# Kernel optimization log

Hardware: AMD Instinct MI355X
Metric: run time of the kernel (lower is better)

The kernel has to match this reference:

```python
import jax, jax.numpy as jnp
import numpy as np

N = 50000      # nodes
E = 800000     # edges (before self loops)
D = 128        # embedding_dimension
HEADS = 4
C = 32         # hidden_channels
NEG_SLOPE = 0.2


def setup_inputs() -> dict:
    key = jax.random.key(0)
    ks = jax.random.split(key, 12)
    s = 0.1
    x = jax.random.normal(ks[0], (N, D), jnp.float32)
    edge_index = jax.random.randint(ks[1], (2, E), 0, N)
    # layer 1: D -> HEADS*C, concat
    W1 = jax.random.normal(ks[2], (D, HEADS * C), jnp.float32) * s
    a_src1 = jax.random.normal(ks[3], (HEADS, C), jnp.float32) * s
    a_dst1 = jax.random.normal(ks[4], (HEADS, C), jnp.float32) * s
    b1 = jnp.zeros((HEADS * C,), jnp.float32)
    # layer 2: HEADS*C -> HEADS*C, concat
    W2 = jax.random.normal(ks[5], (HEADS * C, HEADS * C), jnp.float32) * s
    a_src2 = jax.random.normal(ks[6], (HEADS, C), jnp.float32) * s
    a_dst2 = jax.random.normal(ks[7], (HEADS, C), jnp.float32) * s
    b2 = jnp.zeros((HEADS * C,), jnp.float32)
    # layer 3: HEADS*C -> C, heads=1, no concat (mean over the single head)
    W3 = jax.random.normal(ks[8], (HEADS * C, C), jnp.float32) * s
    a_src3 = jax.random.normal(ks[9], (1, C), jnp.float32) * s
    a_dst3 = jax.random.normal(ks[10], (1, C), jnp.float32) * s
    b3 = jnp.zeros((C,), jnp.float32)
    return {"x": x, "edge_index": edge_index,
            "W1": W1, "a_src1": a_src1, "a_dst1": a_dst1, "b1": b1,
            "W2": W2, "a_src2": a_src2, "a_dst2": a_dst2, "b2": b2,
            "W3": W3, "a_src3": a_src3, "a_dst3": a_dst3, "b3": b3}


def gat_layer(x, src, dst, W, a_s, a_d, b, heads, concat):
    """One PyG-style GATConv (eval mode: dropout inactive).
    x: [N, Fin]; src/dst: [E2] (self loops included)."""
    n = x.shape[0]
    h = (x @ W).reshape(n, heads, -1)                 # [N, H, C]
    alpha_src = (h * a_s).sum(-1)                     # [N, H]
    alpha_dst = (h * a_d).sum(-1)                     # [N, H]
    logits = jax.nn.leaky_relu(alpha_src[src] + alpha_dst[dst], NEG_SLOPE)  # [E2, H]
    # segment softmax over destination nodes
    m = jax.ops.segment_max(logits, dst, num_segments=n)          # [N, H]
    ex = jnp.exp(logits - m[dst])                                  # [E2, H]
    denom = jax.ops.segment_sum(ex, dst, num_segments=n)          # [N, H]
    alpha = ex / (denom[dst] + 1e-16)                              # [E2, H]
    msg = h[src] * alpha[:, :, None]                               # [E2, H, C]
    out = jax.ops.segment_sum(msg, dst, num_segments=n)            # [N, H, C]
    if concat:
        return out.reshape(n, -1) + b
    return out.mean(axis=1) + b


def reference(x, edge_index, W1, a_src1, a_dst1, b1, W2, a_src2, a_dst2, b2,
              W3, a_src3, a_dst3, b3):
    loops = jnp.arange(N, dtype=edge_index.dtype)
    src = jnp.concatenate([edge_index[0], loops])   # add_self_loops=True
    dst = jnp.concatenate([edge_index[1], loops])
    h = gat_layer(x, src, dst, W1, a_src1, a_dst1, b1, HEADS, True)
    h = jax.nn.elu(h)
    h = gat_layer(h, src, dst, W2, a_src2, a_dst2, b2, HEADS, True)
    h = jax.nn.elu(h)
    out = gat_layer(h, src, dst, W3, a_src3, a_dst3, b3, 1, False)
    return out
```

## Files before the change

### kernel.cpp

```cpp
#include <hip/hip_runtime.h>
#include <cmath>

constexpr int NN  = 50000;
constexpr int EE  = 800000;
constexpr int E2C = EE + NN;

constexpr int NBUCK = 256;
constexpr int BW    = 196;
constexpr int NCH   = 16;
constexpr int CW    = 3125;
constexpr int EPT   = 8;
constexpr int CH    = 256 * EPT;
constexpr int NB_B  = (E2C + CH - 1) / CH;
constexpr int CAP   = 4096;
constexpr int SCAP  = 5120;
constexpr int G1ALL = (NN + 63) / 64;
constexpr int G1A   = 391;

constexpr float RLN2 = 1.44269504088896340736f;

using bf16x8 = __attribute__((ext_vector_type(8))) short;
using f32x4  = __attribute__((ext_vector_type(4))) float;

__device__ inline unsigned bf16rne(float f) {
    unsigned u = __builtin_bit_cast(unsigned, f);
    return (u + 0x7fffu + ((u >> 16) & 1u)) >> 16;
}
__device__ inline float bflo(unsigned u) { return __builtin_bit_cast(float, u << 16); }
__device__ inline float bfhi(unsigned u) { return __builtin_bit_cast(float, u & 0xffff0000u); }

__global__ __launch_bounds__(256) void cvt_weights(
    const float* __restrict__ W1, const float* __restrict__ W2,
    const float* __restrict__ W3,
    unsigned short* __restrict__ W1t, unsigned short* __restrict__ W2t,
    unsigned short* __restrict__ W3t, int* __restrict__ bcursor,
    float* __restrict__ AS1, float* __restrict__ AS2, float* __restrict__ AS3,
    unsigned short* __restrict__ H1, unsigned short* __restrict__ H2,
    unsigned short* __restrict__ H3)
{
    int g = blockIdx.x * 256 + threadIdx.x;
    if (g < NBUCK) bcursor[g] = 0;
    if (g < 4) { AS1[NN * 4 + g] = -1e30f; AS2[NN * 4 + g] = -1e30f; }
    if (g == 4) AS3[NN] = -1e30f;
    if (g < 128) { H1[(size_t)NN * 128 + g] = 0; H2[(size_t)NN * 128 + g] = 0; }
    if (g < 32)  H3[(size_t)NN * 32 + g] = 0;

    const float* W; unsigned short* Wt; int cols;
    if (g < 2048)      { W = W1; Wt = W1t; cols = 128; }
    else if (g < 4096) { W = W2; Wt = W2t; cols = 128; g -= 2048; }
    else if (g < 4608) { W = W3; Wt = W3t; cols = 32;  g -= 4096; }
    else return;
    int c  = g / 16;
    int k8 = (g % 16) * 8;
    unsigned up[4];
    #pragma unroll
    for (int j = 0; j < 4; ++j) {
        float a = W[(k8 + 2 * j) * cols + c];
        float b = W[(k8 + 2 * j + 1) * cols + c];
        up[j] = bf16rne(a) | (bf16rne(b) << 16);
    }
    uint4 u; u.x = up[0]; u.y = up[1]; u.z = up[2]; u.w = up[3];
    *(uint4*)(Wt + c * 128 + k8) = u;
}

template<int NT, int NH, bool F32IN>
__device__ inline void gemm_body(
    int bid, const void* __restrict__ inv, const unsigned short* __restrict__ Wt,
    const float* __restrict__ a_s, const float* __restrict__ a_d,
    unsigned short* __restrict__ hout, float* __restrict__ asrc,
    float* __restrict__ adst)
{
    constexpr int COLS = NT * 16;
    constexpr int TPH  = NT / NH;
    const int lane = threadIdx.x & 63;
    const int wave = threadIdx.x >> 6;
    const int m    = lane & 15;
    const int quad = lane >> 4;
    const int n0   = bid * 64 + wave * 16;

    int arow = n0 + m; if (arow >= NN) arow = NN - 1;

    f32x4 acc[NT] = {};
    #pragma unroll
    for (int kq = 0; kq < 4; ++kq) {
        bf16x8 a;
        if constexpr (F32IN) {
            const float* ap = (const float*)inv + (long long)arow * 128 + quad * 8 + kq * 32;
            float4 v0 = *(const float4*)ap;
            float4 v1 = *(const float4*)(ap + 4);
            a[0] = (short)bf16rne(v0.x); a[1] = (short)bf16rne(v0.y);
            a[2] = (short)bf16rne(v0.z); a[3] = (short)bf16rne(v0.w);
            a[4] = (short)bf16rne(v1.x); a[5] = (short)bf16rne(v1.y);
            a[6] = (short)bf16rne(v1.z); a[7] = (short)bf16rne(v1.w);
        } else {
            a = *(const bf16x8*)((const unsigned short*)inv
                    + (long long)arow * 128 + quad * 8 + kq * 32);
        }
        #pragma unroll
        for (int t = 0; t < NT; ++t) {
            bf16x8 b = *(const bf16x8*)(Wt + (t * 16 + m) * 128 + kq * 32 + quad * 8);
            acc[t] = __builtin_amdgcn_mfma_f32_16x16x32_bf16(a, b, acc[t], 0, 0, 0);
        }
    }

    #pragma unroll
    for (int r = 0; r < 4; ++r) {
        int node = n0 + quad * 4 + r;
        if (node < NN) {
            #pragma unroll
            for (int t = 0; t < NT; ++t)
                hout[(long long)node * COLS + t * 16 + m] =
                    (unsigned short)bf16rne(acc[t][r]);
        }
    }

    float asv[NT], adv[NT];
    #pragma unroll
    for (int t = 0; t < NT; ++t) {
        asv[t] = a_s[t * 16 + m] * RLN2;
        adv[t] = a_d[t * 16 + m] * RLN2;
    }

    #pragma unroll
    for (int r = 0; r < 4; ++r) {
        const int node = n0 + quad * 4 + r;
        #pragma unroll
        for (int hh = 0; hh < NH; ++hh) {
            float ps = 0.f, pd = 0.f;
            #pragma unroll
            for (int q = 0; q < TPH; ++q) {
                int t = hh * TPH + q;
                ps = fmaf(acc[t][r], asv[t], ps);
                pd = fmaf(acc[t][r], adv[t], pd);
            }
            #pragma unroll
            for (int off = 8; off > 0; off >>= 1) {
                ps += __shfl_down(ps, off, 16);
                pd += __shfl_down(pd, off, 16);
            }
            if (m == 0 && node < NN) {
                asrc[node * NH + hh] = ps;
                adst[node * NH + hh] = pd;
            }
        }
    }
}

__device__ inline void bin_body(
    int bid, const int* __restrict__ ei, int* __restrict__ bcursor,
    unsigned* __restrict__ pairs)
{
    __shared__ int cnt[NBUCK];
    __shared__ int scanex[NBUCK];
    __shared__ int base[NBUCK];
    __shared__ int cur[NBUCK];
    __shared__ unsigned stage[CH];

    const int tid = threadIdx.x;
    const long long e0 = (long long)bid * CH;
    cnt[tid] = 0;
    __syncthreads();

    unsigned rec[EPT]; int bk[EPT];
    #pragma unroll
    for (int j = 0; j < EPT; ++j) {
        long long e = e0 + tid + j * 256;
        bool valid = e < E2C;
        int ss = 0, dd = 0;
        if (valid) {
            if (e < EE) { ss = ei[e]; dd = ei[EE + e]; }
            else        { ss = dd = (int)(e - EE); }
        }
        int b = dd / BW;
        bk[j]  = valid ? b : -1;
        rec[j] = (unsigned)ss | ((unsigned)(dd - b * BW) << 16) | ((unsigned)b << 24);
        if (valid) atomicAdd(&cnt[b], 1);
    }
    __syncthreads();

    const int myc = cnt[tid];
    scanex[tid] = myc;
    __syncthreads();
    for (int off = 1; off < NBUCK; off <<= 1) {
        int t = (tid >= off) ? scanex[tid - off] : 0;
        __syncthreads();
        scanex[tid] += t;
        __syncthreads();
    }
    int excl = scanex[tid] - myc;
    __syncthreads();
    scanex[tid] = excl;
    cur[tid]    = excl;
    base[tid]   = atomicAdd(&bcursor[tid], myc);
    __syncthreads();

    #pragma unroll
    for (int j = 0; j < EPT; ++j) {
        if (bk[j] >= 0) {
            int p = atomicAdd(&cur[bk[j]], 1);
            stage[p] = rec[j];
        }
    }
    __syncthreads();

    const int total = (e0 + CH <= E2C) ? CH : (int)(E2C - e0);
    for (int j = tid; j < total; j += 256) {
        unsigned p = stage[j];
        int b = (int)(p >> 24);
        pairs[(size_t)b * CAP + base[b] + (j - scanex[b])] = p;
    }
}

__device__ inline void sort_body(
    int b, const int* __restrict__ bcursor, const unsigned* __restrict__ pairs,
    int2* __restrict__ rowp, unsigned short* __restrict__ sorted_src,
    unsigned short* __restrict__ perm)
{
    __shared__ int deg[256];
    __shared__ int scn[256];
    __shared__ int cur[256];
    __shared__ int hist2[64];
    __shared__ int scn2[64];
    __shared__ int cur2[64];
    const int n0 = b * BW;
    const int n1 = (n0 + BW < NN) ? n0 + BW : NN;
    const int nloc = n1 - n0;
    const int tid = threadIdx.x;
    const int mycnt = bcursor[b];
    const unsigned* seg = pairs + (size_t)b * CAP;
    const int base = b * SCAP;

    deg[tid] = 0;
    if (tid < 64) hist2[tid] = 0;
    __syncthreads();
    for (int i = tid; i < mycnt; i += 256)
        atomicAdd(&deg[(seg[i] >> 16) & 0xff], 1);
    __syncthreads();

    const int pv = (deg[tid] + 3) & ~3;
    int it = pv >> 2; if (it > 63) it = 63;
    it = 63 - it;
    scn[tid] = pv;
    if (tid < nloc) atomicAdd(&hist2[it], 1);
    __syncthreads();
    for (int off = 1; off < 256; off <<= 1) {
        int t = (tid >= off) ? scn[tid - off] : 0;
        __syncthreads();
        scn[tid] += t;
        __syncthreads();
    }
    if (tid < 64) scn2[tid] = hist2[tid];
    __syncthreads();
    for (int off = 1; off < 64; off <<= 1) {
        int t = (tid >= off && tid < 64) ? scn2[tid - off] : 0;
        __syncthreads();
        if (tid < 64) scn2[tid] += t;
        __syncthreads();
    }
    if (tid < 64) cur2[tid] = scn2[tid] - hist2[tid];
    __syncthreads();

    const int totalp = scn[255];
    const int pexcl  = scn[tid] - pv;
    cur[tid] = base + pexcl;
    if (tid < nloc) {
        int rank = atomicAdd(&cur2[it], 1);
        perm[n0 + rank] = (unsigned short)(n0 + tid);
        rowp[n0 + rank] = make_int2(base + pexcl, base + pexcl + pv);
    }
    __syncthreads();

    int lim = totalp + 8; if (lim > SCAP) lim = SCAP;
    for (int i = tid; i < lim; i += 256)
        sorted_src[base + i] = (unsigned short)NN;
    if (b == NBUCK - 1 && tid < 8)
        sorted_src[NBUCK * SCAP + tid] = (unsigned short)NN;
    __syncthreads();

    for (int c = 0; c < NCH; ++c) {
        const unsigned lo = (unsigned)(c * CW), hi = lo + CW;
        for (int i = tid; i < mycnt; i += 256) {
            unsigned p = seg[i];
            unsigned ss = p & 0xffffu;
            if (ss >= lo && ss < hi) {
                int pos = atomicAdd(&cur[(p >> 16) & 0xff], 1);
                sorted_src[pos] = (unsigned short)ss;
            }
        }
        __syncthreads();
    }
}

__global__ __launch_bounds__(256) void bin_gemm(
    const int* __restrict__ ei, int* __restrict__ bcursor,
    unsigned* __restrict__ pairs,
    const float* __restrict__ x, const unsigned short* __restrict__ Wt,
    const float* __restrict__ a_s, const float* __restrict__ a_d,
    unsigned short* __restrict__ hout, float* __restrict__ asrc,
    float* __restrict__ adst)
{
    if (blockIdx.x < NB_B)
        bin_body(blockIdx.x, ei, bcursor, pairs);
    else
        gemm_body<8, 4, true>(blockIdx.x - NB_B, x, Wt, a_s, a_d, hout, asrc, adst);
}

__global__ __launch_bounds__(256) void sort_gemm(
    const int* __restrict__ bcursor, const unsigned* __restrict__ pairs,
    int2* __restrict__ rowp, unsigned short* __restrict__ sorted_src,
    unsigned short* __restrict__ perm,
    const float* __restrict__ x, const unsigned short* __restrict__ Wt,
    const float* __restrict__ a_s, const float* __restrict__ a_d,
    unsigned short* __restrict__ hout, float* __restrict__ asrc,
    float* __restrict__ adst)
{
    if (blockIdx.x < NBUCK)
        sort_body(blockIdx.x, bcursor, pairs, rowp, sorted_src, perm);
    else
        gemm_body<8, 4, true>(blockIdx.x - NBUCK + G1A, x, Wt, a_s, a_d,
                              hout, asrc, adst);
}

template<int COLS, int NH>
__device__ inline void aggr_range(
    int b0, int e0, int head, float ad,
    const unsigned short* __restrict__ sorted_src,
    const uint* __restrict__ hp,
    const float* __restrict__ asrc,
    float num[8], float& den)
{
    constexpr int USTR = COLS / 2;
    ushort4 sv = *(const ushort4*)&sorted_src[b0];
    for (int i = b0; i < e0; i += 4) {
        ushort4 nx = *(const ushort4*)&sorted_src[i + 4];
        const int s[4] = {sv.x, sv.y, sv.z, sv.w};
        float a[4];
        uint4 Hv[4];
        #pragma unroll
        for (int j = 0; j < 4; ++j) a[j] = asrc[s[j] * NH + head];
        #pragma unroll
        for (int j = 0; j < 4; ++j)
            Hv[j] = *(const uint4*)&hp[(long long)s[j] * USTR];
        #pragma unroll
        for (int j = 0; j < 4; ++j) {
            float l = a[j] + ad; l = l > 0.f ? l : 0.2f * l;
            float w;
            asm("v_exp_f32 %0, %1" : "=v"(w) : "v"(l));
            den += w;
            num[0] = fmaf(w, bflo(Hv[j].x), num[0]); num[1] = fmaf(w, bfhi(Hv[j].x), num[1]);
            num[2] = fmaf(w, bflo(Hv[j].y), num[2]); num[3] = fmaf(w, bfhi(Hv[j].y), num[3]);
            num[4] = fmaf(w, bflo(Hv[j].z), num[4]); num[5] = fmaf(w, bfhi(Hv[j].z), num[5]);
            num[6] = fmaf(w, bflo(Hv[j].w), num[6]); num[7] = fmaf(w, bfhi(Hv[j].w), num[7]);
        }
        sv = nx;
    }
}

template<int NT_OUT, int NH_OUT>
__global__ __launch_bounds__(256) void aggr_gemm(
    const unsigned short* __restrict__ perm,
    const int2* __restrict__ rowp, const unsigned short* __restrict__ sorted_src,
    const unsigned short* __restrict__ hin,
    const float* __restrict__ asrc_in, const float* __restrict__ adst_in,
    const float* __restrict__ bias,
    const unsigned short* __restrict__ Wt,
    const float* __restrict__ a_s, const float* __restrict__ a_d,
    unsigned short* __restrict__ hout, float* __restrict__ asrc_out,
    float* __restrict__ adst_out)
{
    __shared__ unsigned short lds_h[16 * 128];
    __shared__ int lds_node[16];
    const int tid = threadIdx.x;
    const int row = tid >> 4;
    const int lc  = tid & 15;
    const int rk  = blockIdx.x * 16 + row;
    const int d   = perm[rk];
    if (lc == 0) lds_node[row] = d;

    const int cc   = lc * 8;
    const int head = cc / 32;
    const float ad = adst_in[d * 4 + head];
    const uint* hp = (const uint*)hin + cc / 2;
    const int2 be = rowp[rk];

    float num[8] = {};
    float den = 0.f;
    aggr_range<128, 4>(be.x, be.y, head, ad, sorted_src, hp, asrc_in, num, den);

    float inv = 1.f / (den + 1e-16f);
    float v[8];
    #pragma unroll
    for (int j = 0; j < 8; ++j) {
        v[j] = num[j] * inv + bias[cc + j];
        v[j] = v[j] > 0.f ? v[j] : expm1f(v[j]);
    }
    uint4 u;
    u.x = bf16rne(v[0]) | (bf16rne(v[1]) << 16);
    u.y = bf16rne(v[2]) | (bf16rne(v[3]) << 16);
    u.z = bf16rne(v[4]) | (bf16rne(v[5]) << 16);
    u.w = bf16rne(v[6]) | (bf16rne(v[7]) << 16);
    *(uint4*)((char*)lds_h + row * 256 + ((lc * 16) ^ ((row & 7) << 4))) = u;
    __syncthreads();

    const int lane = tid & 63;
    const int wave = tid >> 6;
    const int m    = lane & 15;
    const int quad = lane >> 4;
    int t0;
    if constexpr (NT_OUT == 8) t0 = wave * 2;
    else { if (wave != 0) return; t0 = 0; }

    f32x4 acc[2] = {};
    #pragma unroll
    for (int kq = 0; kq < 4; ++kq) {
        int colb = (quad * 16 + kq * 64) ^ ((m & 7) << 4);
        bf16x8 a = *(const bf16x8*)((const char*)lds_h + m * 256 + colb);
        #pragma unroll
        for (int tt = 0; tt < 2; ++tt) {
            bf16x8 b = *(const bf16x8*)(Wt + ((t0 + tt) * 16 + m) * 128
                                        + kq * 32 + quad * 8);
            acc[tt] = __builtin_amdgcn_mfma_f32_16x16x32_bf16(a, b, acc[tt], 0, 0, 0);
        }
    }

    constexpr int COLS_OUT = NT_OUT * 16;
    const int headw = t0 / (NT_OUT / NH_OUT);
    float asv[2], adv[2];
    #pragma unroll
    for (int tt = 0; tt < 2; ++tt) {
        asv[tt] = a_s[(t0 + tt) * 16 + m] * RLN2;
        adv[tt] = a_d[(t0 + tt) * 16 + m] * RLN2;
    }

    #pragma unroll
    for (int r = 0; r < 4; ++r) {
        const int node = lds_node[quad * 4 + r];
        #pragma unroll
        for (int tt = 0; tt < 2; ++tt)
            hout[(long long)node * COLS_OUT + (t0 + tt) * 16 + m] =
                (unsigned short)bf16rne(acc[tt][r]);
        float ps = acc[0][r] * asv[0];
        ps = fmaf(acc[1][r], asv[1], ps);
        float pd = acc[0][r] * adv[0];
        pd = fmaf(acc[1][r], adv[1], pd);
        #pragma unroll
        for (int off = 8; off > 0; off >>= 1) {
            ps += __shfl_down(ps, off, 16);
            pd += __shfl_down(pd, off, 16);
        }
        if (m == 0) {
            asrc_out[node * NH_OUT + headw] = ps;
            adst_out[node * NH_OUT + headw] = pd;
        }
    }
}

template<int COLS, int NH>
__global__ __launch_bounds__(256) void aggr_final(
    const unsigned short* __restrict__ perm,
    const int2* __restrict__ rowp, const unsigned short* __restrict__ sorted_src,
    const unsigned short* __restrict__ hin,
    const float* __restrict__ asrc, const float* __restrict__ adst,
    const float* __restrict__ bias, float* __restrict__ out)
{
    constexpr int TPN = COLS / 8;
    int t = blockIdx.x * 256 + threadIdx.x;
    int rk = t / TPN;
    int lc = t % TPN;
    if (rk >= NN) return;
    const int d = perm[rk];
    const int cc = lc * 8;
    const int head = cc / 32;
    const float ad = adst[d * NH + head];
    const int2 be = rowp[rk];
    const uint* hp = (const uint*)hin + cc / 2;
    float num[8] = {};
    float den = 0.f;
    aggr_range<COLS, NH>(be.x, be.y, head, ad, sorted_src, hp, asrc, num, den);
    float inv = 1.f / (den + 1e-16f);
    float v[8];
    #pragma unroll
    for (int j = 0; j < 8; ++j) v[j] = num[j] * inv + bias[cc + j];
    float4 o0 = {v[0], v[1], v[2], v[3]};
    float4 o1 = {v[4], v[5], v[6], v[7]};
    *(float4*)&out[(long long)d * COLS + lc * 8]     = o0;
    *(float4*)&out[(long long)d * COLS + lc * 8 + 4] = o1;
}

extern "C" void kernel_launch(void* const* d_in, const int* in_sizes, int n_in,
                              void* d_out, int out_size, void* d_ws, size_t ws_size,
                              hipStream_t stream)
{
    const float* x   = (const float*)d_in[0];
    const int*   ei  = (const int*)  d_in[1];
    const float* W1  = (const float*)d_in[2];
    const float* as1 = (const float*)d_in[3];
    const float* ad1 = (const float*)d_in[4];
    const float* b1  = (const float*)d_in[5];
    const float* W2  = (const float*)d_in[6];
    const float* as2 = (const float*)d_in[7];
    const float* ad2 = (const float*)d_in[8];
    const float* b2  = (const float*)d_in[9];
    const float* W3  = (const float*)d_in[10];
    const float* as3 = (const float*)d_in[11];
    const float* ad3 = (const float*)d_in[12];
    const float* b3  = (const float*)d_in[13];
    float* out = (float*)d_out;

    unsigned short* H1  = (unsigned short*)d_ws;
    unsigned short* H2  = H1 + (size_t)(NN + 1) * 128;
    unsigned short* H3  = H2 + (size_t)(NN + 1) * 128;
    unsigned short* W1t = H3 + (size_t)(NN + 1) * 32;
    unsigned short* W2t = W1t + 128 * 128;
    unsigned short* W3t = W2t + 128 * 128;
    float* AS1 = (float*)(W3t + 32 * 128);
    float* AD1 = AS1 + (size_t)(NN + 1) * 4;
    float* AS2 = AD1 + (size_t)NN * 4;
    float* AD2 = AS2 + (size_t)(NN + 1) * 4;
    float* AS3 = AD2 + (size_t)NN * 4;
    float* AD3 = AS3 + (size_t)(NN + 1);
    int2* rowp = (int2*)(AD3 + NN);
    unsigned short* sorted = (unsigned short*)(rowp + NN);
    int* bcursor = (int*)(sorted + (size_t)NBUCK * SCAP + 8);
    unsigned short* perm = (unsigned short*)(bcursor + NBUCK);
    size_t off = ((size_t)(perm + NN) - (size_t)d_ws + 15) & ~(size_t)15;
    unsigned* pairs = (unsigned*)((char*)d_ws + off);

    const int gCvtW  = (4608 + 255) / 256;
    const int gBinG  = NB_B + G1A;
    const int gSortG = NBUCK + (G1ALL - G1A);
    const int gFused = NN / 16;
    const int gAggr3 = (NN * 4 + 255) / 256;

    cvt_weights<<<gCvtW, 256, 0, stream>>>(W1, W2, W3, W1t, W2t, W3t, bcursor,
                                           AS1, AS2, AS3, H1, H2, H3);
    bin_gemm<<<gBinG, 256, 0, stream>>>(ei, bcursor, pairs,
                                        x, W1t, as1, ad1, H1, AS1, AD1);
    sort_gemm<<<gSortG, 256, 0, stream>>>(bcursor, pairs, rowp, sorted, perm,
                                          x, W1t, as1, ad1, H1, AS1, AD1);
    aggr_gemm<8, 4><<<gFused, 256, 0, stream>>>(
        perm, rowp, sorted, H1, AS1, AD1, b1, W2t, as2, ad2, H2, AS2, AD2);
    aggr_gemm<2, 1><<<gFused, 256, 0, stream>>>(
        perm, rowp, sorted, H2, AS2, AD2, b2, W3t, as3, ad3, H3, AS3, AD3);
    aggr_final<32, 1><<<gAggr3, 256, 0, stream>>>(
        perm, rowp, sorted, H3, AS3, AD3, b3, out);
}
```

Baseline: 284.6 us.

## Use column-sliced feature layout and split aggregation from GEMM

Hidden features are now stored as column slices (16 or 8 columns per slice, each slice holding all nodes). Aggregation kernels then work on one slice per block, so gathered rows are smaller and the working set fits the cache better. The fused aggregate+GEMM kernels are split into separate slice-wise aggregation and standalone GEMM launches. This adds launches and an extra round trip of intermediates through memory. The sort step also drops its chunked multi-pass scatter for a single pass, which changes the order of source indices within each row.

Result: slower. 351.3 us (+23.4%).

```diff
diff --git a/kernel.cpp b/kernel.cpp
--- a/kernel.cpp
+++ b/kernel.cpp
@@ -7,8 +7,6 @@
 
 constexpr int NBUCK = 256;
 constexpr int BW    = 196;
-constexpr int NCH   = 16;
-constexpr int CW    = 3125;
 constexpr int EPT   = 8;
 constexpr int CH    = 256 * EPT;
 constexpr int NB_B  = (E2C + CH - 1) / CH;
@@ -21,6 +19,7 @@
 
 using bf16x8 = __attribute__((ext_vector_type(8))) short;
 using f32x4  = __attribute__((ext_vector_type(4))) float;
+using u32x4  = __attribute__((ext_vector_type(4))) unsigned int;
 
 __device__ inline unsigned bf16rne(float f) {
     unsigned u = __builtin_bit_cast(unsigned, f);
@@ -35,15 +34,19 @@
     unsigned short* __restrict__ W1t, unsigned short* __restrict__ W2t,
     unsigned short* __restrict__ W3t, int* __restrict__ bcursor,
     float* __restrict__ AS1, float* __restrict__ AS2, float* __restrict__ AS3,
-    unsigned short* __restrict__ H1, unsigned short* __restrict__ H2,
+    unsigned short* __restrict__ HA, unsigned short* __restrict__ HB,
     unsigned short* __restrict__ H3)
 {
     int g = blockIdx.x * 256 + threadIdx.x;
     if (g < NBUCK) bcursor[g] = 0;
     if (g < 4) { AS1[NN * 4 + g] = -1e30f; AS2[NN * 4 + g] = -1e30f; }
     if (g == 4) AS3[NN] = -1e30f;
-    if (g < 128) { H1[(size_t)NN * 128 + g] = 0; H2[(size_t)NN * 128 + g] = 0; }
-    if (g < 32)  H3[(size_t)NN * 32 + g] = 0;
+    if (g < 128) {
+        HA[((size_t)(g >> 4) * (NN + 1) + NN) * 16 + (g & 15)] = 0;
+        HB[((size_t)(g >> 4) * (NN + 1) + NN) * 16 + (g & 15)] = 0;
+    }
+    if (g < 32)
+        H3[((size_t)(g >> 3) * (NN + 1) + NN) * 8 + (g & 7)] = 0;
 
     const float* W; unsigned short* Wt; int cols;
     if (g < 2048)      { W = W1; Wt = W1t; cols = 128; }
@@ -63,7 +66,7 @@
     *(uint4*)(Wt + c * 128 + k8) = u;
 }
 
-template<int NT, int NH, bool F32IN>
+template<int NT, int NH, bool F32IN, int GRP_OUT>
 __device__ inline void gemm_body(
     int bid, const void* __restrict__ inv, const unsigned short* __restrict__ Wt,
     const float* __restrict__ a_s, const float* __restrict__ a_d,
@@ -93,8 +96,9 @@
             a[4] = (short)bf16rne(v1.x); a[5] = (short)bf16rne(v1.y);
             a[6] = (short)bf16rne(v1.z); a[7] = (short)bf16rne(v1.w);
         } else {
+            int c = quad * 8 + kq * 32;
             a = *(const bf16x8*)((const unsigned short*)inv
-                    + (long long)arow * 128 + quad * 8 + kq * 32);
+                    + ((size_t)(c >> 4) * (NN + 1) + arow) * 16 + (c & 15));
         }
         #pragma unroll
         for (int t = 0; t < NT; ++t) {
@@ -108,9 +112,15 @@
         int node = n0 + quad * 4 + r;
         if (node < NN) {
             #pragma unroll
-            for (int t = 0; t < NT; ++t)
-                hout[(long long)node * COLS + t * 16 + m] =
-                    (unsigned short)bf16rne(acc[t][r]);
+            for (int t = 0; t < NT; ++t) {
+                int c2 = t * 16 + m;
+                if constexpr (GRP_OUT == 16)
+                    hout[((size_t)(c2 >> 4) * (NN + 1) + node) * 16 + (c2 & 15)] =
+                        (unsigned short)bf16rne(acc[t][r]);
+                else
+                    hout[((size_t)(c2 >> 3) * (NN + 1) + node) * 8 + (c2 & 7)] =
+                        (unsigned short)bf16rne(acc[t][r]);
+            }
         }
     }
 
@@ -276,18 +286,10 @@
     if (b == NBUCK - 1 && tid < 8)
         sorted_src[NBUCK * SCAP + tid] = (unsigned short)NN;
     __syncthreads();
-
-    for (int c = 0; c < NCH; ++c) {
-        const unsigned lo = (unsigned)(c * CW), hi = lo + CW;
-        for (int i = tid; i < mycnt; i += 256) {
-            unsigned p = seg[i];
-            unsigned ss = p & 0xffffu;
-            if (ss >= lo && ss < hi) {
-                int pos = atomicAdd(&cur[(p >> 16) & 0xff], 1);
-                sorted_src[pos] = (unsigned short)ss;
-            }
-        }
-        __syncthreads();
+    for (int i = tid; i < mycnt; i += 256) {
+        unsigned p = seg[i];
+        int pos = atomicAdd(&cur[(p >> 16) & 0xff], 1);
+        sorted_src[pos] = (unsigned short)(p & 0xffff);
     }
 }
 
@@ -302,7 +304,8 @@
     if (blockIdx.x < NB_B)
         bin_body(blockIdx.x, ei, bcursor, pairs);
     else
-        gemm_body<8, 4, true>(blockIdx.x - NB_B, x, Wt, a_s, a_d, hout, asrc, adst);
+        gemm_body<8, 4, true, 16>(blockIdx.x - NB_B, x, Wt, a_s, a_d,
+                                  hout, asrc, adst);
 }
 
 __global__ __launch_bounds__(256) void sort_gemm(
@@ -317,8 +320,26 @@
     if (blockIdx.x < NBUCK)
         sort_body(blockIdx.x, bcursor, pairs, rowp, sorted_src, perm);
     else
-        gemm_body<8, 4, true>(blockIdx.x - NBUCK + G1A, x, Wt, a_s, a_d,
-                              hout, asrc, adst);
+        gemm_body<8, 4, true, 16>(blockIdx.x - NBUCK + G1A, x, Wt, a_s, a_d,
+                                  hout, asrc, adst);
+}
+
+__global__ __launch_bounds__(256) void gemm_l2(
+    const unsigned short* __restrict__ hin, const unsigned short* __restrict__ Wt,
+    const float* __restrict__ a_s, const float* __restrict__ a_d,
+    unsigned short* __restrict__ hout, float* __restrict__ asrc,
+    float* __restrict__ adst)
+{
+    gemm_body<8, 4, false, 16>(blockIdx.x, hin, Wt, a_s, a_d, hout, asrc, adst);
+}
+
+__global__ __launch_bounds__(256) void gemm_l3(
+    const unsigned short* __restrict__ hin, const unsigned short* __restrict__ Wt,
+    const float* __restrict__ a_s, const float* __restrict__ a_d,
+    unsigned short* __restrict__ hout, float* __restrict__ asrc,
+    float* __restrict__ adst)
+{
+    gemm_body<2, 1, false, 8>(blockIdx.x, hin, Wt, a_s, a_d, hout, asrc, adst);
 }
 
 template<int COLS, int NH>
@@ -356,135 +377,76 @@
     }
 }
 
-template<int NT_OUT, int NH_OUT>
-__global__ __launch_bounds__(256) void aggr_gemm(
+__global__ __launch_bounds__(256) void aggr_slice128(
     const unsigned short* __restrict__ perm,
     const int2* __restrict__ rowp, const unsigned short* __restrict__ sorted_src,
     const unsigned short* __restrict__ hin,
-    const float* __restrict__ asrc_in, const float* __restrict__ adst_in,
+    const float* __restrict__ asrc, const float* __restrict__ adst,
     const float* __restrict__ bias,
-    const unsigned short* __restrict__ Wt,
-    const float* __restrict__ a_s, const float* __restrict__ a_d,
-    unsigned short* __restrict__ hout, float* __restrict__ asrc_out,
-    float* __restrict__ adst_out)
-{
-    __shared__ unsigned short lds_h[16 * 128];
-    __shared__ int lds_node[16];
-    const int tid = threadIdx.x;
-    const int row = tid >> 4;
-    const int lc  = tid & 15;
-    const int rk  = blockIdx.x * 16 + row;
-    const int d   = perm[rk];
-    if (lc == 0) lds_node[row] = d;
-
-    const int cc   = lc * 8;
-    const int head = cc / 32;
-    const float ad = adst_in[d * 4 + head];
-    const uint* hp = (const uint*)hin + cc / 2;
-    const int2 be = rowp[rk];
+    unsigned short* __restrict__ outg)
+{
+    const int g    = blockIdx.x & 7;
+    const int ib   = blockIdx.x >> 3;
+    const int tid  = threadIdx.x;
+    const int ln   = tid >> 1;
+    const int half = tid & 1;
+    const int rk   = ib * 128 + ln;
+    if (rk >= NN) return;
+    const int d    = perm[rk];
+    const int head = g >> 1;
+    const float ad = adst[d * 4 + head];
+    const uint* hp = (const uint*)hin + (size_t)g * (NN + 1) * 8 + half * 4;
+    const int2 be  = rowp[rk];
 
     float num[8] = {};
     float den = 0.f;
-    aggr_range<128, 4>(be.x, be.y, head, ad, sorted_src, hp, asrc_in, num, den);
+    aggr_range<16, 4>(be.x, be.y, head, ad, sorted_src, hp, asrc, num, den);
 
     float inv = 1.f / (den + 1e-16f);
+    const int cc = g * 16 + half * 8;
     float v[8];
     #pragma unroll
     for (int j = 0; j < 8; ++j) {
         v[j] = num[j] * inv + bias[cc + j];
         v[j] = v[j] > 0.f ? v[j] : expm1f(v[j]);
     }
-    uint4 u;
-    u.x = bf16rne(v[0]) | (bf16rne(v[1]) << 16);
-    u.y = bf16rne(v[2]) | (bf16rne(v[3]) << 16);
-    u.z = bf16rne(v[4]) | (bf16rne(v[5]) << 16);
-    u.w = bf16rne(v[6]) | (bf16rne(v[7]) << 16);
-    *(uint4*)((char*)lds_h + row * 256 + ((lc * 16) ^ ((row & 7) << 4))) = u;
-    __syncthreads();
-
-    const int lane = tid & 63;
-    const int wave = tid >> 6;
-    const int m    = lane & 15;
-    const int quad = lane >> 4;
-    int t0;
-    if constexpr (NT_OUT == 8) t0 = wave * 2;
-    else { if (wave != 0) return; t0 = 0; }
-
-    f32x4 acc[2] = {};
-    #pragma unroll
-    for (int kq = 0; kq < 4; ++kq) {
-        int colb = (quad * 16 + kq * 64) ^ ((m & 7) << 4);
-        bf16x8 a = *(const bf16x8*)((const char*)lds_h + m * 256 + colb);
-        #pragma unroll
-        for (int tt = 0; tt < 2; ++tt) {
-            bf16x8 b = *(const bf16x8*)(Wt + ((t0 + tt) * 16 + m) * 128
-                                        + kq * 32 + quad * 8);
-            acc[tt] = __builtin_amdgcn_mfma_f32_16x16x32_bf16(a, b, acc[tt], 0, 0, 0);
-        }
-    }
-
-    constexpr int COLS_OUT = NT_OUT * 16;
-    const int headw = t0 / (NT_OUT / NH_OUT);
-    float asv[2], adv[2];
-    #pragma unroll
-    for (int tt = 0; tt < 2; ++tt) {
-        asv[tt] = a_s[(t0 + tt) * 16 + m] * RLN2;
-        adv[tt] = a_d[(t0 + tt) * 16 + m] * RLN2;
-    }
-
-    #pragma unroll
-    for (int r = 0; r < 4; ++r) {
-        const int node = lds_node[quad * 4 + r];
-        #pragma unroll
-        for (int tt = 0; tt < 2; ++tt)
-            hout[(long long)node * COLS_OUT + (t0 + tt) * 16 + m] =
-                (unsigned short)bf16rne(acc[tt][r]);
-        float ps = acc[0][r] * asv[0];
-        ps = fmaf(acc[1][r], asv[1], ps);
-        float pd = acc[0][r] * adv[0];
-        pd = fmaf(acc[1][r], adv[1], pd);
-        #pragma unroll
-        for (int off = 8; off > 0; off >>= 1) {
-            ps += __shfl_down(ps, off, 16);
-            pd += __shfl_down(pd, off, 16);
-        }
-        if (m == 0) {
-            asrc_out[node * NH_OUT + headw] = ps;
-            adst_out[node * NH_OUT + headw] = pd;
-        }
-    }
-}
-
-template<int COLS, int NH>
-__global__ __launch_bounds__(256) void aggr_final(
+    u32x4 u;
+    u[0] = bf16rne(v[0]) | (bf16rne(v[1]) << 16);
+    u[1] = bf16rne(v[2]) | (bf16rne(v[3]) << 16);
+    u[2] = bf16rne(v[4]) | (bf16rne(v[5]) << 16);
+    u[3] = bf16rne(v[6]) | (bf16rne(v[7]) << 16);
+    __builtin_nontemporal_store(
+        u, (u32x4*)(outg + ((size_t)g * (NN + 1) + d) * 16 + half * 8));
+}
+
+__global__ __launch_bounds__(256) void aggr_final_g(
     const unsigned short* __restrict__ perm,
     const int2* __restrict__ rowp, const unsigned short* __restrict__ sorted_src,
     const unsigned short* __restrict__ hin,
     const float* __restrict__ asrc, const float* __restrict__ adst,
     const float* __restrict__ bias, float* __restrict__ out)
 {
-    constexpr int TPN = COLS / 8;
-    int t = blockIdx.x * 256 + threadIdx.x;
-    int rk = t / TPN;
-    int lc = t % TPN;
+    const int g  = blockIdx.x & 3;
+    const int ib = blockIdx.x >> 2;
+    const int rk = ib * 256 + threadIdx.x;
     if (rk >= NN) return;
-    const int d = perm[rk];
-    const int cc = lc * 8;
-    const int head = cc / 32;
-    const float ad = adst[d * NH + head];
-    const int2 be = rowp[rk];
-    const uint* hp = (const uint*)hin + cc / 2;
+    const int d  = perm[rk];
+    const float ad = adst[d];
+    const uint* hp = (const uint*)hin + (size_t)g * (NN + 1) * 4;
+    const int2 be  = rowp[rk];
+
     float num[8] = {};
     float den = 0.f;
-    aggr_range<COLS, NH>(be.x, be.y, head, ad, sorted_src, hp, asrc, num, den);
+    aggr_range<8, 1>(be.x, be.y, 0, ad, sorted_src, hp, asrc, num, den);
+
     float inv = 1.f / (den + 1e-16f);
+    const int cc = g * 8;
     float v[8];
     #pragma unroll
     for (int j = 0; j < 8; ++j) v[j] = num[j] * inv + bias[cc + j];
-    float4 o0 = {v[0], v[1], v[2], v[3]};
-    float4 o1 = {v[4], v[5], v[6], v[7]};
-    *(float4*)&out[(long long)d * COLS + lc * 8]     = o0;
-    *(float4*)&out[(long long)d * COLS + lc * 8 + 4] = o1;
+    float* op = out + (long long)d * 32 + cc;
+    *(float4*)(op)     = make_float4(v[0], v[1], v[2], v[3]);
+    *(float4*)(op + 4) = make_float4(v[4], v[5], v[6], v[7]);
 }
 
 extern "C" void kernel_launch(void* const* d_in, const int* in_sizes, int n_in,
@@ -507,9 +469,9 @@
     const float* b3  = (const float*)d_in[13];
     float* out = (float*)d_out;
 
-    unsigned short* H1  = (unsigned short*)d_ws;
-    unsigned short* H2  = H1 + (size_t)(NN + 1) * 128;
-    unsigned short* H3  = H2 + (size_t)(NN + 1) * 128;
+    unsigned short* HA  = (unsigned short*)d_ws;
+    unsigned short* HB  = HA + (size_t)(NN + 1) * 128;
+    unsigned short* H3  = HB + (size_t)(NN + 1) * 128;
     unsigned short* W1t = H3 + (size_t)(NN + 1) * 32;
     unsigned short* W2t = W1t + 128 * 128;
     unsigned short* W3t = W2t + 128 * 128;
@@ -529,19 +491,22 @@
     const int gCvtW  = (4608 + 255) / 256;
     const int gBinG  = NB_B + G1A;
     const int gSortG = NBUCK + (G1ALL - G1A);
-    const int gFused = NN / 16;
-    const int gAggr3 = (NN * 4 + 255) / 256;
+    const int gGemm  = G1ALL;
+    const int gAggrS = 8 * ((NN + 127) / 128);
+    const int gAggrF = 4 * ((NN + 255) / 256);
 
     cvt_weights<<<gCvtW, 256, 0, stream>>>(W1, W2, W3, W1t, W2t, W3t, bcursor,
-                                           AS1, AS2, AS3, H1, H2, H3);
+                                           AS1, AS2, AS3, HA, HB, H3);
     bin_gemm<<<gBinG, 256, 0, stream>>>(ei, bcursor, pairs,
-                                        x, W1t, as1, ad1, H1, AS1, AD1);
+                                        x, W1t, as1, ad1, HA, AS1, AD1);
     sort_gemm<<<gSortG, 256, 0, stream>>>(bcursor, pairs, rowp, sorted, perm,
-                                          x, W1t, as1, ad1, H1, AS1, AD1);
-    aggr_gemm<8, 4><<<gFused, 256, 0, stream>>>(
-        perm, rowp, sorted, H1, AS1, AD1, b1, W2t, as2, ad2, H2, AS2, AD2);
-    aggr_gemm<2, 1><<<gFused, 256, 0, stream>>>(
-        perm, rowp, sorted, H2, AS2, AD2, b2, W3t, as3, ad3, H3, AS3, AD3);
-    aggr_final<32, 1><<<gAggr3, 256, 0, stream>>>(
+                                          x, W1t, as1, ad1, HA, AS1, AD1);
+    aggr_slice128<<<gAggrS, 256, 0, stream>>>(
+        perm, rowp, sorted, HA, AS1, AD1, b1, HB);
+    gemm_l2<<<gGemm, 256, 0, stream>>>(HB, W2t, as2, ad2, HA, AS2, AD2);
+    aggr_slice128<<<gAggrS, 256, 0, stream>>>(
+        perm, rowp, sorted, HA, AS2, AD2, b2, HB);
+    gemm_l3<<<gGemm, 256, 0, stream>>>(HB, W3t, as3, ad3, H3, AS3, AD3);
+    aggr_final_g<<<gAggrF, 256, 0, stream>>>(
         perm, rowp, sorted, H3, AS3, AD3, b3, out);
 }
```
